# Optimization experiments

Hardware: AMD Instinct MI355X
Metric: run time of the kernel (lower is better)

## Reference

```python
import math
import jax, jax.numpy as jnp
import numpy as np

N_NODES = 50000
N_EDGES = 800000
F_IN = 512
HID = 64
N_CLS = 64
NITER = 10


def setup_inputs() -> dict:
    key = jax.random.key(0)
    k = jax.random.split(key, 6)
    x = jax.random.normal(k[0], (N_NODES, F_IN), jnp.float32)
    edge_index = jax.random.randint(k[1], (2, N_EDGES), 0, N_NODES, jnp.int64)
    W1 = jax.random.normal(k[2], (F_IN, HID), jnp.float32) / np.sqrt(F_IN)
    b1 = jnp.zeros((HID,), jnp.float32)
    W2 = jax.random.normal(k[3], (HID, N_CLS), jnp.float32) / np.sqrt(HID)
    b2 = jnp.zeros((N_CLS,), jnp.float32)
    halt_w = jax.random.normal(k[4], (N_CLS,), jnp.float32) / np.sqrt(N_CLS)
    # reset_parameters: bias = log((1/(niter+1)) / (1 - 1/(niter+1)))
    b = math.log((1.0 / (NITER + 1)) / (1.0 - 1.0 / (NITER + 1)))
    halt_b = jnp.full((1,), b, jnp.float32)
    return {"x": x, "edge_index": edge_index, "W1": W1, "b1": b1,
            "W2": W2, "b2": b2, "halt_w": halt_w, "halt_b": halt_b}


def reference(x, edge_index, W1, b1, W2, b2, halt_w, halt_b):
    N = x.shape[0]
    # MLP (eval mode: dropout is identity)
    h = jnp.maximum(x @ W1 + b1, 0.0)
    local = h @ W2 + b2                      # [N, C] local predictions
    # GCN normalization with self-loops (eval: no edge dropout)
    loops = jnp.arange(N, dtype=edge_index.dtype)
    row = jnp.concatenate([edge_index[0], loops])
    col = jnp.concatenate([edge_index[1], loops])
    deg = jnp.zeros((N,), x.dtype).at[row].add(1.0)
    dis = jnp.where(deg > 0, jax.lax.rsqrt(jnp.maximum(deg, 1.0)), 0.0)
    norm = dis[row] * dis[col]               # [E+N]

    def step(carry, _):
        prop, steps, sum_h, cont, xacc = carry
        old = prop
        msg = norm[:, None] * prop[row]                       # gather + scale
        prop = jax.ops.segment_sum(msg, col, num_segments=N)  # scatter-add
        hh = jax.nn.sigmoid(prop @ halt_w + halt_b[0])        # [N]
        prob = (sum_h + hh < 0.99) & cont
        pf = prob.astype(x.dtype)
        steps = steps + pf
        sum_h = sum_h + pf * hh
        cond = prob & (steps < NITER)
        p = jnp.where(cond, sum_h, 1.0 - sum_h)
        xacc = xacc + (prop * p[:, None] + old * (1.0 - p)[:, None]) * cont.astype(x.dtype)[:, None]
        cont = cont & prob
        return (prop, steps, sum_h, cont, xacc), None

    init = (local, jnp.ones((N,), x.dtype), jnp.zeros((N,), x.dtype),
            jnp.ones((N,), bool), jnp.zeros_like(local))
    (prop, steps, sum_h, cont, xacc), _ = jax.lax.scan(step, init, None, length=NITER)
    out = xacc / steps[:, None]
    return jax.nn.log_softmax(out, axis=1), steps, 1.0 - sum_h
```

## Files before the change

### kernel.cpp

```cpp
#include <hip/hip_runtime.h>
#include <hip/hip_bf16.h>

#define F_IN 512
#define NC 64
#define NITER 10
#define BM 128

typedef float fvec4 __attribute__((ext_vector_type(4)));

__global__ __launch_bounds__(256) void mlp_kernel(
    const float* __restrict__ x, const float* __restrict__ W1,
    const float* __restrict__ b1, const float* __restrict__ W2,
    const float* __restrict__ b2, float* __restrict__ out, int N) {
  __shared__ float xs[BM * NC];
  __shared__ float ws[NC * NC];
  const int tid  = threadIdx.x;
  const int brow = blockIdx.x * BM;
  const int rg = tid >> 4;
  const int cg = tid & 15;
  const int r0 = rg * 8;
  const int c0 = cg * 4;
  const int keyr = rg & 7;

  float acc[8][4];
#pragma unroll
  for (int j = 0; j < 4; ++j) {
    float bv = b1[c0 + j];
#pragma unroll
    for (int i = 0; i < 8; ++i) acc[i][j] = bv;
  }

  for (int kt = 0; kt < F_IN; kt += 64) {
#pragma unroll
    for (int q = 0; q < 8; ++q) {
      int c = q * 256 + tid;
      int row = c >> 4, kc = c & 15;
      int gr = brow + row; if (gr >= N) gr = N - 1;
      float4 v = *reinterpret_cast<const float4*>(&x[(size_t)gr * F_IN + kt + kc * 4]);
      *reinterpret_cast<float4*>(&xs[row * NC + ((kc ^ ((row >> 3) & 7)) << 2)]) = v;
    }
#pragma unroll
    for (int q = 0; q < 4; ++q) {
      int c = q * 256 + tid;
      *reinterpret_cast<float4*>(&ws[c * 4]) =
          *reinterpret_cast<const float4*>(&W1[(size_t)kt * NC + c * 4]);
    }
    __syncthreads();
#pragma unroll 4
    for (int kc = 0; kc < 16; ++kc) {
      float4 xq[8];
#pragma unroll
      for (int i = 0; i < 8; ++i)
        xq[i] = *reinterpret_cast<const float4*>(&xs[(r0 + i) * NC + ((kc ^ keyr) << 2)]);
#pragma unroll
      for (int m = 0; m < 4; ++m) {
        float4 wv = *reinterpret_cast<const float4*>(&ws[(kc * 4 + m) * NC + c0]);
        float wr[4] = {wv.x, wv.y, wv.z, wv.w};
#pragma unroll
        for (int i = 0; i < 8; ++i) {
          float xm = reinterpret_cast<const float*>(&xq[i])[m];
#pragma unroll
          for (int j = 0; j < 4; ++j) acc[i][j] = fmaf(xm, wr[j], acc[i][j]);
        }
      }
    }
    __syncthreads();
  }

#pragma unroll
  for (int i = 0; i < 8; ++i) {
    float4 hv = make_float4(fmaxf(acc[i][0], 0.f), fmaxf(acc[i][1], 0.f),
                            fmaxf(acc[i][2], 0.f), fmaxf(acc[i][3], 0.f));
    *reinterpret_cast<float4*>(&xs[(r0 + i) * NC + ((cg ^ keyr) << 2)]) = hv;
  }
#pragma unroll
  for (int q = 0; q < 4; ++q) {
    int c = q * 256 + tid;
    *reinterpret_cast<float4*>(&ws[c * 4]) =
        *reinterpret_cast<const float4*>(&W2[c * 4]);
  }
  float acc2[8][4];
#pragma unroll
  for (int j = 0; j < 4; ++j) {
    float bv = b2[c0 + j];
#pragma unroll
    for (int i = 0; i < 8; ++i) acc2[i][j] = bv;
  }
  __syncthreads();
#pragma unroll 4
  for (int kc = 0; kc < 16; ++kc) {
    float4 xq[8];
#pragma unroll
    for (int i = 0; i < 8; ++i)
      xq[i] = *reinterpret_cast<const float4*>(&xs[(r0 + i) * NC + ((kc ^ keyr) << 2)]);
#pragma unroll
    for (int m = 0; m < 4; ++m) {
      float4 wv = *reinterpret_cast<const float4*>(&ws[(kc * 4 + m) * NC + c0]);
      float wr[4] = {wv.x, wv.y, wv.z, wv.w};
#pragma unroll
      for (int i = 0; i < 8; ++i) {
        float xm = reinterpret_cast<const float*>(&xq[i])[m];
#pragma unroll
        for (int j = 0; j < 4; ++j) acc2[i][j] = fmaf(xm, wr[j], acc2[i][j]);
      }
    }
  }
#pragma unroll
  for (int i = 0; i < 8; ++i) {
    int gr = brow + r0 + i;
    if (gr < N) {
      fvec4 o = {acc2[i][0], acc2[i][1], acc2[i][2], acc2[i][3]};
      __builtin_nontemporal_store(o, reinterpret_cast<fvec4*>(&out[(size_t)gr * NC + c0]));
    }
  }
}

__global__ __launch_bounds__(256) void hist_kernel(
    const int* __restrict__ ei, int* __restrict__ deg_i,
    int* __restrict__ indeg, int E) {
  int e = blockIdx.x * blockDim.x + threadIdx.x;
  if (e < E) {
    atomicAdd(&deg_i[ei[e]], 1);
    atomicAdd(&indeg[ei[E + e]], 1);
  }
}

__device__ __forceinline__ int pad8(int v) { return (v + 7) & ~7; }

__global__ __launch_bounds__(256) void scan_sum_kernel(
    const int* __restrict__ indeg, int* __restrict__ bsum,
    const int* __restrict__ deg_i, float* __restrict__ dis, int N) {
  __shared__ int sm[256];
  int tid = threadIdx.x;
  int i = blockIdx.x * 256 + tid;
  sm[tid] = (i < N) ? pad8(indeg[i]) : 0;
  if (i < N) dis[i] = 1.0f / sqrtf((float)(deg_i[i] + 1));
  __syncthreads();
  for (int s = 128; s > 0; s >>= 1) {
    if (tid < s) sm[tid] += sm[tid + s];
    __syncthreads();
  }
  if (tid == 0) bsum[blockIdx.x] = sm[0];
}

__global__ __launch_bounds__(256) void scan_bsum_kernel(int* __restrict__ bsum, int nb) {
  __shared__ int sm[256];
  int tid = threadIdx.x;
  int v = (tid < nb) ? bsum[tid] : 0;
  sm[tid] = v;
  __syncthreads();
  for (int s = 1; s < 256; s <<= 1) {
    int t = (tid >= s) ? sm[tid - s] : 0;
    __syncthreads();
    sm[tid] += t;
    __syncthreads();
  }
  if (tid < nb) bsum[tid] = sm[tid] - v;
}

__global__ __launch_bounds__(256) void scan_final_kernel(
    const int* __restrict__ indeg, const int* __restrict__ bsum,
    int* __restrict__ rowptr, int N) {
  __shared__ int sm[256];
  int tid = threadIdx.x;
  int i = blockIdx.x * 256 + tid;
  int v = (i < N) ? pad8(indeg[i]) : 0;
  sm[tid] = v;
  __syncthreads();
  for (int s = 1; s < 256; s <<= 1) {
    int t = (tid >= s) ? sm[tid - s] : 0;
    __syncthreads();
    sm[tid] += t;
    __syncthreads();
  }
  if (i < N) {
    rowptr[i] = bsum[blockIdx.x] + sm[tid] - v;
    if (i == N - 1) rowptr[N] = bsum[blockIdx.x] + sm[tid];
  }
}

__global__ __launch_bounds__(256) void scatter_kernel(
    const int* __restrict__ ei, const int* __restrict__ rowptr,
    int* __restrict__ cursor, const float* __restrict__ dis,
    int2* __restrict__ csr, int E) {
  int e = blockIdx.x * blockDim.x + threadIdx.x;
  if (e < E) {
    int s = ei[e];
    int c = ei[E + e];
    int pos = rowptr[c] + atomicAdd(&cursor[c], 1);
    csr[pos] = make_int2(s, __float_as_int(dis[s] * dis[c]));
  }
}

__global__ __launch_bounds__(256) void pad_fill_kernel(
    const int* __restrict__ rowptr, const int* __restrict__ indeg,
    int2* __restrict__ csr, int N) {
  int i = blockIdx.x * blockDim.x + threadIdx.x;
  if (i < N) {
    int e = rowptr[i] + indeg[i];
    int end = rowptr[i + 1];
    for (; e < end; ++e) csr[e] = make_int2(0, 0);
  }
}

template<bool FIRST, bool LAST>
__global__ __launch_bounds__(256) void prop_step_kernel(
    const float* __restrict__ prop, float* __restrict__ prop_new,
    const int2* __restrict__ csr, const int* __restrict__ rowptr,
    const float* __restrict__ dis, const float* __restrict__ hw,
    const float* __restrict__ hb, float* __restrict__ steps,
    float* __restrict__ sumh, int* __restrict__ cont,
    float* __restrict__ xacc, float* __restrict__ out0,
    float* __restrict__ out1, float* __restrict__ out2, int N) {
  int wid = (int)((blockIdx.x * blockDim.x + threadIdx.x) >> 6);
  if (wid >= N) return;
  int lane = threadIdx.x & 63;
  size_t rowoff = (size_t)wid * NC + lane;

  float oldv = prop[rowoff];
  float dc = dis[wid];
  int beg = __builtin_amdgcn_readfirstlane(rowptr[wid]);
  int end = __builtin_amdgcn_readfirstlane(rowptr[wid + 1]);

  float a[8];
  a[0] = dc * dc * oldv;
#pragma unroll
  for (int u = 1; u < 8; ++u) a[u] = 0.0f;
  for (int i = beg; i < end; i += 8) {
    int2 e[8];
#pragma unroll
    for (int u = 0; u < 8; ++u) e[u] = csr[i + u];
#pragma unroll
    for (int u = 0; u < 8; ++u)
      a[u] = fmaf(__int_as_float(e[u].y), prop[(size_t)e[u].x * NC + lane], a[u]);
  }
  float acc = ((a[0] + a[1]) + (a[2] + a[3])) + ((a[4] + a[5]) + (a[6] + a[7]));
  if (!LAST) prop_new[rowoff] = acc;

  float z = acc * hw[lane];
#pragma unroll
  for (int off = 32; off > 0; off >>= 1) z += __shfl_xor(z, off);
  z += hb[0];
  float hh = 1.0f / (1.0f + expf(-z));

  float st, sh; int ct;
  if (FIRST) { st = 1.0f; sh = 0.0f; ct = 1; }
  else { st = steps[wid]; sh = sumh[wid]; ct = cont[wid]; }
  bool prob = ((sh + hh) < 0.99f) && (ct != 0);
  float pf = prob ? 1.0f : 0.0f;
  st += pf;
  sh += pf * hh;
  bool cond = prob && (st < (float)NITER);
  float pp = cond ? sh : (1.0f - sh);

  if (!LAST) {
    if (ct != 0) {
      float xa = FIRST ? 0.0f : xacc[rowoff];
      xacc[rowoff] = xa + (acc * pp + oldv * (1.0f - pp));
      if (lane == 0) { steps[wid] = st; sumh[wid] = sh; cont[wid] = prob ? 1 : 0; }
    }
  } else {
    float xa = xacc[rowoff];
    float xnew = (ct != 0) ? xa + (acc * pp + oldv * (1.0f - pp)) : xa;
    float v = xnew / st;
    float m = v;
#pragma unroll
    for (int off = 32; off > 0; off >>= 1) m = fmaxf(m, __shfl_xor(m, off));
    float e = expf(v - m);
    float s = e;
#pragma unroll
    for (int off = 32; off > 0; off >>= 1) s += __shfl_xor(s, off);
    __builtin_nontemporal_store(v - m - logf(s), &out0[rowoff]);
    if (lane == 0) {
      __builtin_nontemporal_store(st, &out1[wid]);
      __builtin_nontemporal_store(1.0f - sh, &out2[wid]);
    }
  }
}

extern "C" void kernel_launch(void* const* d_in, const int* in_sizes, int n_in,
                              void* d_out, int out_size, void* d_ws, size_t ws_size,
                              hipStream_t stream) {
  const float* x      = (const float*)d_in[0];
  const int*   ei     = (const int*)d_in[1];
  const float* W1     = (const float*)d_in[2];
  const float* b1     = (const float*)d_in[3];
  const float* W2     = (const float*)d_in[4];
  const float* b2     = (const float*)d_in[5];
  const float* halt_w = (const float*)d_in[6];
  const float* halt_b = (const float*)d_in[7];

  const int N = in_sizes[0] / F_IN;
  const int E = in_sizes[1] / 2;
  const int EP = E + 8 * N;

  char* p = (char*)d_ws;
  auto alloc = [&](size_t bytes) {
    void* r = (void*)p;
    p += (bytes + 255) & ~(size_t)255;
    return r;
  };
  float* propA  = (float*)alloc((size_t)N * NC * 4);
  float* propB  = (float*)alloc((size_t)N * NC * 4);
  float* xacc   = (float*)alloc((size_t)N * NC * 4);
  int2*  csr    = (int2*)alloc((size_t)EP * 8);
  int*   rowptr = (int*)alloc((size_t)(N + 1) * 4);
  int*   deg_i  = (int*)alloc((size_t)N * 4);
  int*   indeg  = (int*)alloc((size_t)N * 4);
  int*   cursor = (int*)alloc((size_t)N * 4);
  float* dis    = (float*)alloc((size_t)N * 4);
  float* steps  = (float*)alloc((size_t)N * 4);
  float* sumh   = (float*)alloc((size_t)N * 4);
  int*   cont   = (int*)alloc((size_t)N * 4);
  int*   bsum   = (int*)alloc(1024);

  hipMemsetAsync(deg_i,  0, (size_t)N * 4, stream);
  hipMemsetAsync(indeg,  0, (size_t)N * 4, stream);
  hipMemsetAsync(cursor, 0, (size_t)N * 4, stream);

  const int nbN = (N + 255) / 256;
  const int nbE = (E + 255) / 256;
  const int nbM = (N + BM - 1) / BM;

  mlp_kernel<<<nbM, 256, 0, stream>>>(x, W1, b1, W2, b2, propA, N);
  hist_kernel<<<nbE, 256, 0, stream>>>(ei, deg_i, indeg, E);
  scan_sum_kernel<<<nbN, 256, 0, stream>>>(indeg, bsum, deg_i, dis, N);
  scan_bsum_kernel<<<1, 256, 0, stream>>>(bsum, nbN);
  scan_final_kernel<<<nbN, 256, 0, stream>>>(indeg, bsum, rowptr, N);
  scatter_kernel<<<nbE, 256, 0, stream>>>(ei, rowptr, cursor, dis, csr, E);
  pad_fill_kernel<<<nbN, 256, 0, stream>>>(rowptr, indeg, csr, N);

  float* out0 = (float*)d_out;
  float* out1 = out0 + (size_t)N * NC;
  float* out2 = out1 + N;

  const int nbW = (N + 3) / 4;
  const float* cur = propA;
  float* nxt = propB;
  prop_step_kernel<true, false><<<nbW, 256, 0, stream>>>(
      cur, nxt, csr, rowptr, dis, halt_w, halt_b, steps, sumh, cont, xacc,
      out0, out1, out2, N);
  { const float* t = nxt; nxt = (float*)cur; cur = t; }
  for (int it = 1; it < NITER - 1; ++it) {
    prop_step_kernel<false, false><<<nbW, 256, 0, stream>>>(
        cur, nxt, csr, rowptr, dis, halt_w, halt_b, steps, sumh, cont, xacc,
        out0, out1, out2, N);
    const float* t = nxt; nxt = (float*)cur; cur = t;
  }
  prop_step_kernel<false, true><<<nbW, 256, 0, stream>>>(
      cur, nxt, csr, rowptr, dis, halt_w, halt_b, steps, sumh, cont, xacc,
      out0, out1, out2, N);
}
```

Before: 556.5 us.

## Shrink CSR to source indices, compute edge norm on the fly, prefetch MLP tiles

The CSR now stores only the source index (4 bytes instead of 8). Each edge's normalization is rebuilt in the propagation loop from dis[src]*dis[dst], and padding entries point to a zero sentinel row N in prop and dis. This halves CSR traffic in each of the ten propagation steps, at the cost of an extra gather of dis per edge. Separately, the MLP kernel prefetches the next x/W1 tile (and W2) into registers while computing the current one, which overlaps global loads with FMA work but raises register pressure.

```diff
diff --git a/kernel.cpp b/kernel.cpp
--- a/kernel.cpp
+++ b/kernel.cpp
@@ -22,6 +22,23 @@
   const int c0 = cg * 4;
   const int keyr = rg & 7;
 
+  const int srow = tid >> 4;
+  float4 xreg[8];
+  float4 wreg[4];
+
+#pragma unroll
+  for (int q = 0; q < 8; ++q) {
+    int c = q * 256 + tid;
+    int row = c >> 4, kc = c & 15;
+    int gr = brow + row; if (gr >= N) gr = N - 1;
+    xreg[q] = *reinterpret_cast<const float4*>(&x[(size_t)gr * F_IN + kc * 4]);
+  }
+#pragma unroll
+  for (int q = 0; q < 4; ++q) {
+    int c = q * 256 + tid;
+    wreg[q] = *reinterpret_cast<const float4*>(&W1[c * 4]);
+  }
+
   float acc[8][4];
 #pragma unroll
   for (int j = 0; j < 4; ++j) {
@@ -35,17 +52,35 @@
     for (int q = 0; q < 8; ++q) {
       int c = q * 256 + tid;
       int row = c >> 4, kc = c & 15;
-      int gr = brow + row; if (gr >= N) gr = N - 1;
-      float4 v = *reinterpret_cast<const float4*>(&x[(size_t)gr * F_IN + kt + kc * 4]);
-      *reinterpret_cast<float4*>(&xs[row * NC + ((kc ^ ((row >> 3) & 7)) << 2)]) = v;
+      *reinterpret_cast<float4*>(&xs[row * NC + ((kc ^ ((row >> 3) & 7)) << 2)]) = xreg[q];
     }
 #pragma unroll
     for (int q = 0; q < 4; ++q) {
       int c = q * 256 + tid;
-      *reinterpret_cast<float4*>(&ws[c * 4]) =
-          *reinterpret_cast<const float4*>(&W1[(size_t)kt * NC + c * 4]);
-    }
-    __syncthreads();
+      *reinterpret_cast<float4*>(&ws[c * 4]) = wreg[q];
+    }
+    __syncthreads();
+
+    bool more = (kt + 64) < F_IN;
+    if (more) {
+#pragma unroll
+      for (int q = 0; q < 8; ++q) {
+        int c = q * 256 + tid;
+        int row = c >> 4, kc = c & 15;
+        int gr = brow + row; if (gr >= N) gr = N - 1;
+        xreg[q] = *reinterpret_cast<const float4*>(
+            &x[(size_t)gr * F_IN + (kt + 64) + kc * 4]);
+      }
+    }
+    {
+      const float* Wnext = more ? &W1[(size_t)(kt + 64) * NC] : W2;
+#pragma unroll
+      for (int q = 0; q < 4; ++q) {
+        int c = q * 256 + tid;
+        wreg[q] = *reinterpret_cast<const float4*>(&Wnext[c * 4]);
+      }
+    }
+
 #pragma unroll 4
     for (int kc = 0; kc < 16; ++kc) {
       float4 xq[8];
@@ -76,8 +111,7 @@
 #pragma unroll
   for (int q = 0; q < 4; ++q) {
     int c = q * 256 + tid;
-    *reinterpret_cast<float4*>(&ws[c * 4]) =
-        *reinterpret_cast<const float4*>(&W2[c * 4]);
+    *reinterpret_cast<float4*>(&ws[c * 4]) = wreg[q];
   }
   float acc2[8][4];
 #pragma unroll
@@ -135,6 +169,7 @@
   int i = blockIdx.x * 256 + tid;
   sm[tid] = (i < N) ? pad8(indeg[i]) : 0;
   if (i < N) dis[i] = 1.0f / sqrtf((float)(deg_i[i] + 1));
+  if (i == N) dis[N] = 0.0f;
   __syncthreads();
   for (int s = 128; s > 0; s >>= 1) {
     if (tid < s) sm[tid] += sm[tid + s];
@@ -181,32 +216,36 @@
 
 __global__ __launch_bounds__(256) void scatter_kernel(
     const int* __restrict__ ei, const int* __restrict__ rowptr,
-    int* __restrict__ cursor, const float* __restrict__ dis,
-    int2* __restrict__ csr, int E) {
+    int* __restrict__ cursor, int* __restrict__ csr, int E) {
   int e = blockIdx.x * blockDim.x + threadIdx.x;
   if (e < E) {
     int s = ei[e];
     int c = ei[E + e];
     int pos = rowptr[c] + atomicAdd(&cursor[c], 1);
-    csr[pos] = make_int2(s, __float_as_int(dis[s] * dis[c]));
+    csr[pos] = s;
   }
 }
 
 __global__ __launch_bounds__(256) void pad_fill_kernel(
     const int* __restrict__ rowptr, const int* __restrict__ indeg,
-    int2* __restrict__ csr, int N) {
+    int* __restrict__ csr, float* __restrict__ propA,
+    float* __restrict__ propB, int N) {
   int i = blockIdx.x * blockDim.x + threadIdx.x;
+  if (blockIdx.x == 0 && threadIdx.x < NC) {
+    propA[(size_t)N * NC + threadIdx.x] = 0.0f;
+    propB[(size_t)N * NC + threadIdx.x] = 0.0f;
+  }
   if (i < N) {
     int e = rowptr[i] + indeg[i];
     int end = rowptr[i + 1];
-    for (; e < end; ++e) csr[e] = make_int2(0, 0);
+    for (; e < end; ++e) csr[e] = N;
   }
 }
 
 template<bool FIRST, bool LAST>
 __global__ __launch_bounds__(256) void prop_step_kernel(
     const float* __restrict__ prop, float* __restrict__ prop_new,
-    const int2* __restrict__ csr, const int* __restrict__ rowptr,
+    const int* __restrict__ csr, const int* __restrict__ rowptr,
     const float* __restrict__ dis, const float* __restrict__ hw,
     const float* __restrict__ hb, float* __restrict__ steps,
     float* __restrict__ sumh, int* __restrict__ cont,
@@ -227,12 +266,15 @@
 #pragma unroll
   for (int u = 1; u < 8; ++u) a[u] = 0.0f;
   for (int i = beg; i < end; i += 8) {
-    int2 e[8];
-#pragma unroll
-    for (int u = 0; u < 8; ++u) e[u] = csr[i + u];
+    int src[8];
+#pragma unroll
+    for (int u = 0; u < 8; ++u) src[u] = csr[i + u];
+    float dsrc[8];
+#pragma unroll
+    for (int u = 0; u < 8; ++u) dsrc[u] = dis[src[u]];
 #pragma unroll
     for (int u = 0; u < 8; ++u)
-      a[u] = fmaf(__int_as_float(e[u].y), prop[(size_t)e[u].x * NC + lane], a[u]);
+      a[u] = fmaf(dsrc[u] * dc, prop[(size_t)src[u] * NC + lane], a[u]);
   }
   float acc = ((a[0] + a[1]) + (a[2] + a[3])) + ((a[4] + a[5]) + (a[6] + a[7]));
   if (!LAST) prop_new[rowoff] = acc;
@@ -300,15 +342,15 @@
     p += (bytes + 255) & ~(size_t)255;
     return r;
   };
-  float* propA  = (float*)alloc((size_t)N * NC * 4);
-  float* propB  = (float*)alloc((size_t)N * NC * 4);
+  float* propA  = (float*)alloc((size_t)(N + 1) * NC * 4);
+  float* propB  = (float*)alloc((size_t)(N + 1) * NC * 4);
   float* xacc   = (float*)alloc((size_t)N * NC * 4);
-  int2*  csr    = (int2*)alloc((size_t)EP * 8);
+  int*   csr    = (int*)alloc((size_t)EP * 4);
   int*   rowptr = (int*)alloc((size_t)(N + 1) * 4);
   int*   deg_i  = (int*)alloc((size_t)N * 4);
   int*   indeg  = (int*)alloc((size_t)N * 4);
   int*   cursor = (int*)alloc((size_t)N * 4);
-  float* dis    = (float*)alloc((size_t)N * 4);
+  float* dis    = (float*)alloc((size_t)(N + 1) * 4);
   float* steps  = (float*)alloc((size_t)N * 4);
   float* sumh   = (float*)alloc((size_t)N * 4);
   int*   cont   = (int*)alloc((size_t)N * 4);
@@ -327,8 +369,8 @@
   scan_sum_kernel<<<nbN, 256, 0, stream>>>(indeg, bsum, deg_i, dis, N);
   scan_bsum_kernel<<<1, 256, 0, stream>>>(bsum, nbN);
   scan_final_kernel<<<nbN, 256, 0, stream>>>(indeg, bsum, rowptr, N);
-  scatter_kernel<<<nbE, 256, 0, stream>>>(ei, rowptr, cursor, dis, csr, E);
-  pad_fill_kernel<<<nbN, 256, 0, stream>>>(rowptr, indeg, csr, N);
+  scatter_kernel<<<nbE, 256, 0, stream>>>(ei, rowptr, cursor, csr, E);
+  pad_fill_kernel<<<nbN, 256, 0, stream>>>(rowptr, indeg, csr, propA, propB, N);
 
   float* out0 = (float*)d_out;
   float* out1 = out0 + (size_t)N * NC;
```

After: 573.5 us. 3.1% more time.

## Split propagation into chunked-feature gather and separate halting state kernel

Applied to the files above, without the earlier changes.

Stores the propagated features in four column chunks of 16 floats, each with a padding row, so every gathered neighbor row is a 64-byte segment and each chunk's working set is smaller and more cache-friendly. The CSR now holds only source indices, and the edge norm is recomputed from dis. Padding entries point to a zero sentinel node instead of carrying a zero weight. Each iteration now runs a gather kernel and a separate state/halting kernel, so there are twice as many launches and an extra global read of both prop buffers per step.

```diff
diff --git a/kernel.cpp b/kernel.cpp
--- a/kernel.cpp
+++ b/kernel.cpp
@@ -7,6 +7,7 @@
 #define BM 128
 
 typedef float fvec4 __attribute__((ext_vector_type(4)));
+
 
 __global__ __launch_bounds__(256) void mlp_kernel(
     const float* __restrict__ x, const float* __restrict__ W1,
@@ -110,7 +111,8 @@
     int gr = brow + r0 + i;
     if (gr < N) {
       fvec4 o = {acc2[i][0], acc2[i][1], acc2[i][2], acc2[i][3]};
-      __builtin_nontemporal_store(o, reinterpret_cast<fvec4*>(&out[(size_t)gr * NC + c0]));
+      size_t dsto = (size_t)(cg >> 2) * (N + 1) * 16 + (size_t)gr * 16 + (c0 & 15);
+      __builtin_nontemporal_store(o, reinterpret_cast<fvec4*>(&out[dsto]));
     }
   }
 }
@@ -135,6 +137,7 @@
   int i = blockIdx.x * 256 + tid;
   sm[tid] = (i < N) ? pad8(indeg[i]) : 0;
   if (i < N) dis[i] = 1.0f / sqrtf((float)(deg_i[i] + 1));
+  if (i == N) dis[N] = 0.0f;
   __syncthreads();
   for (int s = 128; s > 0; s >>= 1) {
     if (tid < s) sm[tid] += sm[tid + s];
@@ -181,61 +184,85 @@
 
 __global__ __launch_bounds__(256) void scatter_kernel(
     const int* __restrict__ ei, const int* __restrict__ rowptr,
-    int* __restrict__ cursor, const float* __restrict__ dis,
-    int2* __restrict__ csr, int E) {
+    int* __restrict__ cursor, int* __restrict__ csr, int E) {
   int e = blockIdx.x * blockDim.x + threadIdx.x;
   if (e < E) {
     int s = ei[e];
     int c = ei[E + e];
     int pos = rowptr[c] + atomicAdd(&cursor[c], 1);
-    csr[pos] = make_int2(s, __float_as_int(dis[s] * dis[c]));
+    csr[pos] = s;
   }
 }
 
 __global__ __launch_bounds__(256) void pad_fill_kernel(
     const int* __restrict__ rowptr, const int* __restrict__ indeg,
-    int2* __restrict__ csr, int N) {
+    int* __restrict__ csr, float* __restrict__ propA,
+    float* __restrict__ propB, int N) {
   int i = blockIdx.x * blockDim.x + threadIdx.x;
+  if (blockIdx.x == 0 && threadIdx.x < NC) {
+    int c = threadIdx.x >> 4, f = threadIdx.x & 15;
+    size_t o = (size_t)c * (N + 1) * 16 + (size_t)N * 16 + f;
+    propA[o] = 0.0f;
+    propB[o] = 0.0f;
+  }
   if (i < N) {
     int e = rowptr[i] + indeg[i];
     int end = rowptr[i + 1];
-    for (; e < end; ++e) csr[e] = make_int2(0, 0);
-  }
+    for (; e < end; ++e) csr[e] = N;
+  }
+}
+
+__global__ __launch_bounds__(256) void gather_kernel(
+    const float* __restrict__ cur, float* __restrict__ nxt,
+    const int* __restrict__ csr, const int* __restrict__ rowptr,
+    const float* __restrict__ dis, int N) {
+  int chunk = blockIdx.x & 3;
+  int nb = blockIdx.x >> 2;
+  int sg = threadIdx.x >> 4;
+  int lf = threadIdx.x & 15;
+  int node = nb * 16 + sg;
+  if (node >= N) return;
+  const float* curC = cur + (size_t)chunk * (N + 1) * 16;
+  float dc = dis[node];
+  int beg = rowptr[node], end = rowptr[node + 1];
+  size_t off = (size_t)node * 16 + lf;
+
+  float a[8];
+  a[0] = dc * dc * curC[off];
+#pragma unroll
+  for (int u = 1; u < 8; ++u) a[u] = 0.0f;
+  for (int i = beg; i < end; i += 8) {
+    int src[8];
+#pragma unroll
+    for (int u = 0; u < 8; ++u)
+      src[u] = __builtin_nontemporal_load(&csr[i + u]);
+    float ds[8];
+#pragma unroll
+    for (int u = 0; u < 8; ++u) ds[u] = dis[src[u]];
+#pragma unroll
+    for (int u = 0; u < 8; ++u)
+      a[u] = fmaf(ds[u] * dc, curC[(size_t)src[u] * 16 + lf], a[u]);
+  }
+  float acc = ((a[0] + a[1]) + (a[2] + a[3])) + ((a[4] + a[5]) + (a[6] + a[7]));
+  nxt[(size_t)chunk * (N + 1) * 16 + off] = acc;
 }
 
 template<bool FIRST, bool LAST>
-__global__ __launch_bounds__(256) void prop_step_kernel(
-    const float* __restrict__ prop, float* __restrict__ prop_new,
-    const int2* __restrict__ csr, const int* __restrict__ rowptr,
-    const float* __restrict__ dis, const float* __restrict__ hw,
-    const float* __restrict__ hb, float* __restrict__ steps,
-    float* __restrict__ sumh, int* __restrict__ cont,
-    float* __restrict__ xacc, float* __restrict__ out0,
-    float* __restrict__ out1, float* __restrict__ out2, int N) {
+__global__ __launch_bounds__(256) void state_kernel(
+    const float* __restrict__ cur, const float* __restrict__ nxt,
+    const float* __restrict__ hw, const float* __restrict__ hb,
+    float* __restrict__ steps, float* __restrict__ sumh,
+    int* __restrict__ cont, float* __restrict__ xacc,
+    float* __restrict__ out0, float* __restrict__ out1,
+    float* __restrict__ out2, int N) {
   int wid = (int)((blockIdx.x * blockDim.x + threadIdx.x) >> 6);
   if (wid >= N) return;
   int lane = threadIdx.x & 63;
-  size_t rowoff = (size_t)wid * NC + lane;
-
-  float oldv = prop[rowoff];
-  float dc = dis[wid];
-  int beg = __builtin_amdgcn_readfirstlane(rowptr[wid]);
-  int end = __builtin_amdgcn_readfirstlane(rowptr[wid + 1]);
-
-  float a[8];
-  a[0] = dc * dc * oldv;
-#pragma unroll
-  for (int u = 1; u < 8; ++u) a[u] = 0.0f;
-  for (int i = beg; i < end; i += 8) {
-    int2 e[8];
-#pragma unroll
-    for (int u = 0; u < 8; ++u) e[u] = csr[i + u];
-#pragma unroll
-    for (int u = 0; u < 8; ++u)
-      a[u] = fmaf(__int_as_float(e[u].y), prop[(size_t)e[u].x * NC + lane], a[u]);
-  }
-  float acc = ((a[0] + a[1]) + (a[2] + a[3])) + ((a[4] + a[5]) + (a[6] + a[7]));
-  if (!LAST) prop_new[rowoff] = acc;
+  size_t choff = (size_t)(lane >> 4) * (N + 1) * 16 + (lane & 15);
+  size_t nodeoff = (size_t)wid * 16;
+
+  float acc  = nxt[choff + nodeoff];
+  float oldv = cur[choff + nodeoff];
 
   float z = acc * hw[lane];
 #pragma unroll
@@ -252,6 +279,7 @@
   sh += pf * hh;
   bool cond = prob && (st < (float)NITER);
   float pp = cond ? sh : (1.0f - sh);
+  size_t rowoff = (size_t)wid * NC + lane;
 
   if (!LAST) {
     if (ct != 0) {
@@ -300,15 +328,15 @@
     p += (bytes + 255) & ~(size_t)255;
     return r;
   };
-  float* propA  = (float*)alloc((size_t)N * NC * 4);
-  float* propB  = (float*)alloc((size_t)N * NC * 4);
+  float* propA  = (float*)alloc((size_t)(N + 1) * NC * 4);
+  float* propB  = (float*)alloc((size_t)(N + 1) * NC * 4);
   float* xacc   = (float*)alloc((size_t)N * NC * 4);
-  int2*  csr    = (int2*)alloc((size_t)EP * 8);
+  int*   csr    = (int*)alloc((size_t)EP * 4);
   int*   rowptr = (int*)alloc((size_t)(N + 1) * 4);
   int*   deg_i  = (int*)alloc((size_t)N * 4);
   int*   indeg  = (int*)alloc((size_t)N * 4);
   int*   cursor = (int*)alloc((size_t)N * 4);
-  float* dis    = (float*)alloc((size_t)N * 4);
+  float* dis    = (float*)alloc((size_t)(N + 1) * 4);
   float* steps  = (float*)alloc((size_t)N * 4);
   float* sumh   = (float*)alloc((size_t)N * 4);
   int*   cont   = (int*)alloc((size_t)N * 4);
@@ -321,14 +349,15 @@
   const int nbN = (N + 255) / 256;
   const int nbE = (E + 255) / 256;
   const int nbM = (N + BM - 1) / BM;
+  const int nbG = ((N + 15) / 16) * 4;
 
   mlp_kernel<<<nbM, 256, 0, stream>>>(x, W1, b1, W2, b2, propA, N);
   hist_kernel<<<nbE, 256, 0, stream>>>(ei, deg_i, indeg, E);
   scan_sum_kernel<<<nbN, 256, 0, stream>>>(indeg, bsum, deg_i, dis, N);
   scan_bsum_kernel<<<1, 256, 0, stream>>>(bsum, nbN);
   scan_final_kernel<<<nbN, 256, 0, stream>>>(indeg, bsum, rowptr, N);
-  scatter_kernel<<<nbE, 256, 0, stream>>>(ei, rowptr, cursor, dis, csr, E);
-  pad_fill_kernel<<<nbN, 256, 0, stream>>>(rowptr, indeg, csr, N);
+  scatter_kernel<<<nbE, 256, 0, stream>>>(ei, rowptr, cursor, csr, E);
+  pad_fill_kernel<<<nbN, 256, 0, stream>>>(rowptr, indeg, csr, propA, propB, N);
 
   float* out0 = (float*)d_out;
   float* out1 = out0 + (size_t)N * NC;
@@ -337,17 +366,17 @@
   const int nbW = (N + 3) / 4;
   const float* cur = propA;
   float* nxt = propB;
-  prop_step_kernel<true, false><<<nbW, 256, 0, stream>>>(
-      cur, nxt, csr, rowptr, dis, halt_w, halt_b, steps, sumh, cont, xacc,
-      out0, out1, out2, N);
-  { const float* t = nxt; nxt = (float*)cur; cur = t; }
-  for (int it = 1; it < NITER - 1; ++it) {
-    prop_step_kernel<false, false><<<nbW, 256, 0, stream>>>(
-        cur, nxt, csr, rowptr, dis, halt_w, halt_b, steps, sumh, cont, xacc,
-        out0, out1, out2, N);
+  for (int it = 0; it < NITER; ++it) {
+    gather_kernel<<<nbG, 256, 0, stream>>>(cur, nxt, csr, rowptr, dis, N);
+    if (it == 0)
+      state_kernel<true, false><<<nbW, 256, 0, stream>>>(
+          cur, nxt, halt_w, halt_b, steps, sumh, cont, xacc, out0, out1, out2, N);
+    else if (it == NITER - 1)
+      state_kernel<false, true><<<nbW, 256, 0, stream>>>(
+          cur, nxt, halt_w, halt_b, steps, sumh, cont, xacc, out0, out1, out2, N);
+    else
+      state_kernel<false, false><<<nbW, 256, 0, stream>>>(
+          cur, nxt, halt_w, halt_b, steps, sumh, cont, xacc, out0, out1, out2, N);
     const float* t = nxt; nxt = (float*)cur; cur = t;
   }
-  prop_step_kernel<false, true><<<nbW, 256, 0, stream>>>(
-      cur, nxt, csr, rowptr, dis, halt_w, halt_b, steps, sumh, cont, xacc,
-      out0, out1, out2, N);
-}
+}
```

New measurement: 876.7 us. 1.58x slower.
